# Kernel tuning notes

Measured on AMD Instinct MI355X. Metric: run time of the kernel, lower is better.

## Reference

```python
import jax, jax.numpy as jnp
import numpy as np
from jax import lax


def conv2d(x, w, b=None, pad=0):
    y = lax.conv_general_dilated(x, w, (1, 1), [(pad, pad), (pad, pad)],
                                 dimension_numbers=('NCHW', 'OIHW', 'NCHW'))
    if b is not None:
        y = y + b[None, :, None, None]
    return y


def setup_inputs():
    key = jax.random.key(0)
    ks = jax.random.split(key, 8)
    B, C, H, W = 8, 3, 224, 224
    OC, NH, HD = 32, 8, 4
    s = lambda fan: 1.0 / np.sqrt(fan)
    x = jax.random.normal(ks[0], (B, C, H, W), jnp.float32)
    # gumbel noise for the hard gumbel-softmax over attention logits [B,NH,HD,H,H]
    gumbel = jax.random.gumbel(ks[1], (B, NH, HD, H, H), jnp.float32)
    in_w = jax.random.normal(ks[2], (OC, C, 3, 3), jnp.float32) * s(C * 9)
    in_b = jnp.zeros((OC,), jnp.float32)
    qkv_w = jax.random.normal(ks[3], (3 * OC, OC, 3, 3), jnp.float32) * s(OC * 9)
    proj_w = jax.random.normal(ks[4], (OC, OC, 1, 1), jnp.float32) * s(OC)
    proj_b = jnp.zeros((OC,), jnp.float32)
    upd_w = jax.random.normal(ks[5], (OC, OC, 1, 1), jnp.float32) * s(OC)
    upd_b = jnp.zeros((OC,), jnp.float32)
    bn_gamma = jnp.ones((OC,), jnp.float32)
    bn_beta = jnp.zeros((OC,), jnp.float32)
    return {"x": x, "gumbel": gumbel, "in_w": in_w, "in_b": in_b, "qkv_w": qkv_w,
            "proj_w": proj_w, "proj_b": proj_b, "upd_w": upd_w, "upd_b": upd_b,
            "bn_gamma": bn_gamma, "bn_beta": bn_beta}


def reference(x, gumbel, in_w, in_b, qkv_w, proj_w, proj_b, upd_w, upd_b, bn_gamma, bn_beta):
    B, _, H, W = x.shape
    NH, HD = 8, 4
    OC = NH * HD
    EPS = 1e-5
    x1 = conv2d(x, in_w, in_b, pad=1)                       # [B,32,H,W]
    qkv = conv2d(x1, qkv_w, None, pad=1).reshape(B, NH, 3, HD, H, W)
    q, k, v = qkv[:, :, 0], qkv[:, :, 1], qkv[:, :, 2]      # each [B,NH,HD,H,W]
    scale = HD ** -0.5
    # matmul(q, k^T) over the last two dims -> [B,NH,HD,H,H]
    logits = jnp.einsum('bndiw,bndjw->bndij', q, k) * scale
    # hard gumbel-softmax, tau=1, straight-through
    y_soft = jax.nn.softmax(logits + gumbel, axis=-1)
    idx = jnp.argmax(y_soft, axis=-1)
    y_hard = jax.nn.one_hot(idx, H, dtype=y_soft.dtype)
    att = y_hard - lax.stop_gradient(y_soft) + y_soft
    A = jnp.einsum('bndij,bndjw->bndiw', att, v).reshape(B, OC, H, W)
    # F.interpolate to (224,224) bilinear is identity since H=W=224
    A = conv2d(A, proj_w, proj_b)
    A = conv2d(A, upd_w, upd_b)
    # BatchNorm2d in training mode (batch statistics, biased variance)
    mean = A.mean(axis=(0, 2, 3), keepdims=True)
    var = ((A - mean) ** 2).mean(axis=(0, 2, 3), keepdims=True)
    A = (A - mean) * lax.rsqrt(var + EPS)
    A = A * bn_gamma[None, :, None, None] + bn_beta[None, :, None, None]
    A = A * jax.nn.sigmoid(A)  # SiLU; dropout is identity (eval)
    out = A + x1
    return out, att
```

## Files before the change

### kernel.cpp

```cpp
#include <hip/hip_runtime.h>
#include <hip/hip_bf16.h>

#define NB 8
#define CIN 3
#define HH 224
#define WW 224
#define OC 32
#define NH 8
#define HD 4
#define NHD 32
#define C96 96
#define HWSZ (HH*WW)

#define PH 226
#define PW 228
#define CHS (PH*PW)

#define HT 4
#define OCT 8
#define NGB 4


__device__ __forceinline__ void gld_lds16(const float* gsrc, float* ldst) {
    __builtin_amdgcn_global_load_lds(
        (const __attribute__((address_space(1))) uint32_t*)gsrc,
        (__attribute__((address_space(3))) uint32_t*)ldst,
        16, 0, 0);
}

__global__ void k_w2(const float* __restrict__ pw, const float* __restrict__ pb,
                     const float* __restrict__ uw, const float* __restrict__ ub,
                     float* __restrict__ W2, float* __restrict__ b2) {
    int c = threadIdx.x, o = threadIdx.y;
    float acc = 0.f;
    for (int m = 0; m < OC; ++m) acc = fmaf(uw[o*OC + m], pw[m*OC + c], acc);
    W2[o*OC + c] = acc;
    if (c == 0) {
        float bb = ub[o];
        for (int m = 0; m < OC; ++m) bb = fmaf(uw[o*OC + m], pb[m], bb);
        b2[o] = bb;
    }
}

__global__ __launch_bounds__(256) void k_conv_in_tile(const float* __restrict__ x,
                                                      const float* __restrict__ w,
                                                      const float* __restrict__ bias,
                                                      float* __restrict__ x1) {
    int h0 = blockIdx.x * 2;
    int b  = blockIdx.y;
    __shared__ float xs[CIN][4][226];
    int t = threadIdx.x;
    for (int ch = 0; ch < CIN; ++ch)
        for (int r = 0; r < 4; ++r) {
            int gh = h0 - 1 + r;
            for (int col = t; col < 226; col += 256) {
                float v = 0.f;
                if (gh >= 0 && gh < HH && col > 0 && col < 225)
                    v = x[((size_t)(b*CIN + ch)*HH + gh)*WW + (col-1)];
                xs[ch][r][col] = v;
            }
        }
    __syncthreads();
    int wv = t;
    if (wv >= WW) return;
    float xv[CIN][4][3];
    #pragma unroll
    for (int c = 0; c < CIN; ++c)
        #pragma unroll
        for (int r = 0; r < 4; ++r)
            #pragma unroll
            for (int j = 0; j < 3; ++j)
                xv[c][r][j] = xs[c][r][wv + j];
    float acc[2][OC];
    #pragma unroll
    for (int hy = 0; hy < 2; ++hy)
        for (int oc = 0; oc < OC; ++oc) acc[hy][oc] = 0.f;
    #pragma unroll
    for (int c = 0; c < CIN; ++c)
        #pragma unroll
        for (int kh = 0; kh < 3; ++kh)
            #pragma unroll
            for (int kw = 0; kw < 3; ++kw)
                for (int oc = 0; oc < OC; ++oc) {
                    float wgt = w[oc*CIN*9 + c*9 + kh*3 + kw];
                    #pragma unroll
                    for (int hy = 0; hy < 2; ++hy)
                        acc[hy][oc] = fmaf(xv[c][hy+kh][kw], wgt, acc[hy][oc]);
                }
    for (int oc = 0; oc < OC; ++oc) {
        float bs = bias[oc];
        #pragma unroll
        for (int hy = 0; hy < 2; ++hy)
            x1[((size_t)(b*OC + oc)*PH + (h0+hy+1))*PW + (wv+1)] = __fadd_rn(acc[hy][oc], bs);
    }
}

__global__ __launch_bounds__(256) void k_conv_qkv_tile(const float* __restrict__ x1g,
                                                       const float* __restrict__ w,
                                                       float* __restrict__ qk4,
                                                       float* __restrict__ vbg) {
    int h0 = blockIdx.x * HT;
    int og = blockIdx.y * OCT;
    int z  = blockIdx.z;
    const float* x1b = x1g + (size_t)z*OC*CHS;
    float* qk = qk4 + (size_t)z*64*HWSZ;
    float* vb = vbg + (size_t)z*OC*HWSZ;
    __shared__ float xs[2][2240];
    int t = threadIdx.x;
    int lane = t & 63, wid = t >> 6;
    int wv = t;
    float acc[HT][OCT];
    #pragma unroll
    for (int a = 0; a < HT; ++a)
        #pragma unroll
        for (int o = 0; o < OCT; ++o) acc[a][o] = 0.f;

    {
        const float* src = x1b + (size_t)h0*PW;
        for (int k = wid; k < 6; k += 4)
            gld_lds16(src + k*256 + lane*4, &xs[0][k*256]);
    }
    __syncthreads();

    for (int c = 0; c < OC; ++c) {
        int cur = c & 1;
        if (c + 1 < OC) {
            const float* src = x1b + (size_t)(c+1)*CHS + (size_t)h0*PW;
            float* dst = xs[cur ^ 1];
            for (int k = wid; k < 6; k += 4)
                gld_lds16(src + k*256 + lane*4, dst + k*256);
        }
        if (wv < WW) {
            float xv[HT+2][3];
            #pragma unroll
            for (int r = 0; r < HT+2; ++r)
                #pragma unroll
                for (int j = 0; j < 3; ++j)
                    xv[r][j] = xs[cur][r*PW + wv + j];
            #pragma unroll
            for (int o = 0; o < OCT; ++o) {
                const float* wr = w + ((size_t)(og + o)*OC + c)*9;
                #pragma unroll
                for (int kh = 0; kh < 3; ++kh)
                    #pragma unroll
                    for (int kw = 0; kw < 3; ++kw) {
                        float wgt = wr[kh*3 + kw];
                        #pragma unroll
                        for (int hy = 0; hy < HT; ++hy)
                            acc[hy][o] = fmaf(xv[hy+kh][kw], wgt, acc[hy][o]);
                    }
            }
        }
        __syncthreads();
    }
    if (wv < WW) {
        #pragma unroll
        for (int o = 0; o < OCT; ++o) {
            int oc = og + o;
            int rem = oc % 12;
            int r = rem >> 2, d = rem & 3;
            int n = oc / 12;
            if (r == 0) {
                #pragma unroll
                for (int hy = 0; hy < HT; ++hy)
                    qk[((size_t)(n*8 + d)*HH + (h0+hy))*WW + wv] = acc[hy][o];
            } else if (r == 2) {
                #pragma unroll
                for (int hy = 0; hy < HT; ++hy)
                    vb[((size_t)(n*4 + d)*HH + (h0+hy))*WW + wv] = acc[hy][o];
            }
        }
    }
    int ogm = og % 12;
    if (ogm != 8) {
        int ko = (ogm == 0) ? 4 : 0;
        int n  = og / 12;
        float* kt = &xs[0][0];
        if (wv < WW) {
            int wb = wv >> 2, wl = wv & 3;
            #pragma unroll
            for (int kk = 0; kk < 4; ++kk)
                #pragma unroll
                for (int hy = 0; hy < HT; ++hy)
                    kt[(kk*56 + wb)*20 + hy*4 + wl] = acc[hy][ko + kk];
        }
        __syncthreads();
        if (wv < WW) {
            int wb = wv >> 2, s = wv & 3;
            #pragma unroll
            for (int kk = 0; kk < 4; ++kk) {
                float4 kvv = *(const float4*)(&kt[(kk*56 + wb)*20 + s*4]);
                *(float4*)(qk + (size_t)(n*8 + 4 + kk)*HWSZ
                               + (size_t)wb*(HH*4) + (size_t)(h0 + s)*4) = kvv;
            }
        }
    }
}

__global__ __launch_bounds__(256) void k_attn_ri(const float* __restrict__ qk4,
                                                 const float* __restrict__ gum,
                                                 float* __restrict__ att,
                                                 int* __restrict__ idxout,
                                                 int b0) {
    int i0 = blockIdx.x * 8;
    int nd = blockIdx.y;
    int z  = blockIdx.z;
    int b  = b0 + z;
    const float* qkz = qk4 + (size_t)z*64*HWSZ;
    const float* gumb = gum + (size_t)b*NHD*HH*HH;
    float* attb = att + (size_t)b*NHD*HH*HH;
    int* idxb = idxout + (size_t)b*NHD*HH;
    int n = nd >> 2, d = nd & 3;
    const float* qb = qkz + ((size_t)(n*8 + d)*HH + i0)*WW;
    const float* kT = qkz + (size_t)(n*8 + 4 + d)*HWSZ;
    __shared__ __align__(16) float qs[8][WW];
    __shared__ float vals[8][256];
    __shared__ int   win_s[8];
    int t = threadIdx.x;
    for (int f = t; f < 8*(WW/4); f += 256) {
        int r = f / (WW/4), p = (f % (WW/4))*4;
        *(float4*)(&qs[r][p]) = *(const float4*)(qb + (size_t)r*WW + p);
    }
    __syncthreads();
    if (t < WW) {
        float s0[8], s1[8], s2[8], s3[8];
        #pragma unroll
        for (int ii = 0; ii < 8; ++ii) { s0[ii]=0.f; s1[ii]=0.f; s2[ii]=0.f; s3[ii]=0.f; }
        const float* kTt = kT + (size_t)t*4;
        for (int w = 0; w < WW; w += 4) {
            float4 kc = *(const float4*)(kTt + (size_t)(w >> 2)*(HH*4));
            #pragma unroll
            for (int ii = 0; ii < 8; ++ii) {
                float4 qc = *(const float4*)(&qs[ii][w]);
                s0[ii] = __fadd_rn(s0[ii], __fmul_rn(qc.x, kc.x));
                s1[ii] = __fadd_rn(s1[ii], __fmul_rn(qc.y, kc.y));
                s2[ii] = __fadd_rn(s2[ii], __fmul_rn(qc.z, kc.z));
                s3[ii] = __fadd_rn(s3[ii], __fmul_rn(qc.w, kc.w));
            }
        }
        #pragma unroll
        for (int ii = 0; ii < 8; ++ii) {
            float dot = __fadd_rn(__fadd_rn(s0[ii], s1[ii]), __fadd_rn(s2[ii], s3[ii]));
            vals[ii][t] = __fadd_rn(__fmul_rn(0.5f, dot),
                                    gumb[((size_t)nd*HH + (i0 + ii))*HH + t]);
        }
    } else {
        #pragma unroll
        for (int ii = 0; ii < 8; ++ii) vals[ii][t] = -INFINITY;
    }
    __syncthreads();
    int ii = t >> 5, jj = t & 31;
    float best = -INFINITY; int bj = 0x7fffffff;
    for (int j = jj; j < 256; j += 32) {
        float v = vals[ii][j];
        if (v > best) { best = v; bj = j; }
    }
    for (int off = 16; off > 0; off >>= 1) {
        float v2 = __shfl_down(best, off, 32);
        int   j2 = __shfl_down(bj,   off, 32);
        if (v2 > best || (v2 == best && j2 < bj)) { best = v2; bj = j2; }
    }
    if (jj == 0) { win_s[ii] = bj; idxb[nd*HH + i0 + ii] = bj; }
    __syncthreads();
    for (int e = t; e < 8*WW; e += 256) {
        int r = e / WW, j = e - r*WW;
        attb[((size_t)nd*HH + (i0 + r))*HH + j] = (j == win_s[r]) ? 1.f : 0.f;
    }
}

__global__ __launch_bounds__(256) void k_gather_mm(const float* __restrict__ vbuf,
                                                   const int* __restrict__ idx,
                                                   const float* __restrict__ W2g,
                                                   const float* __restrict__ b2g,
                                                   float* __restrict__ A2) {
    int i = blockIdx.x, b = blockIdx.y;
    __shared__ float w2s[OC*OC];
    __shared__ float b2s[OC];
    __shared__ int   id[OC];
    for (int t = threadIdx.x; t < OC*OC; t += blockDim.x) w2s[t] = W2g[t];
    if (threadIdx.x < OC) {
        b2s[threadIdx.x] = b2g[threadIdx.x];
        id[threadIdx.x]  = idx[(b*NHD + threadIdx.x)*HH + i];
    }
    __syncthreads();
    int wv = threadIdx.x;
    if (wv >= WW) return;
    float vals[OC];
    for (int c = 0; c < OC; ++c)
        vals[c] = vbuf[((size_t)(b*OC + c)*HH + id[c])*WW + wv];
    for (int oc = 0; oc < OC; ++oc) {
        float a = b2s[oc];
        for (int c = 0; c < OC; ++c) a = fmaf(w2s[oc*OC + c], vals[c], a);
        A2[((size_t)(b*OC + oc)*HH + i)*WW + wv] = a;
    }
}

__global__ __launch_bounds__(256) void k_stats(const float* __restrict__ A2,
                                               float* __restrict__ sums,
                                               float* __restrict__ sumsq) {
    int oc = blockIdx.x, s = blockIdx.y;
    int t = threadIdx.x;
    float a = 0.f, a2 = 0.f;
    const int SL = HWSZ/16;
    for (int b = 0; b < NB; ++b) {
        const float* base = A2 + (size_t)(b*OC + oc)*HWSZ + s*SL;
        for (int e = t*4; e < SL; e += 256*4) {
            float4 v = *(const float4*)(base + e);
            a  += v.x + v.y + v.z + v.w;
            a2 += v.x*v.x + v.y*v.y + v.z*v.z + v.w*v.w;
        }
    }
    __shared__ float r1[256], r2[256];
    r1[t] = a; r2[t] = a2;
    __syncthreads();
    for (int st = 128; st > 0; st >>= 1) {
        if (t < st) { r1[t] += r1[t+st]; r2[t] += r2[t+st]; }
        __syncthreads();
    }
    if (t == 0) { atomicAdd(&sums[oc], r1[0]); atomicAdd(&sumsq[oc], r2[0]); }
}

__global__ __launch_bounds__(256) void k_final(const float* __restrict__ A2,
                                               const float* __restrict__ x1,
                                               const float* __restrict__ sums,
                                               const float* __restrict__ sumsq,
                                               const float* __restrict__ gamma,
                                               const float* __restrict__ beta,
                                               float* __restrict__ out) {
    int i = blockIdx.x, b = blockIdx.y;
    __shared__ float mean_s[OC], inv_s[OC], g_s[OC], be_s[OC];
    if (threadIdx.x < OC) {
        int oc = threadIdx.x;
        const float N = (float)(NB*HH*WW);
        float mean = sums[oc]/N;
        float var  = sumsq[oc]/N - mean*mean;
        mean_s[oc] = mean;
        inv_s[oc]  = rsqrtf(var + 1e-5f);
        g_s[oc]    = gamma[oc];
        be_s[oc]   = beta[oc];
    }
    __syncthreads();
    int wv = threadIdx.x;
    if (wv >= WW) return;
    for (int oc = 0; oc < OC; ++oc) {
        size_t o = ((size_t)(b*OC + oc)*HH + i)*WW + wv;
        float a = A2[o];
        float an = (a - mean_s[oc])*inv_s[oc]*g_s[oc] + be_s[oc];
        float sw = an / (1.f + __expf(-an));
        out[o] = sw + x1[((size_t)(b*OC + oc)*PH + (i+1))*PW + (wv+1)];
    }
}

extern "C" void kernel_launch(void* const* d_in, const int* in_sizes, int n_in,
                              void* d_out, int out_size, void* d_ws, size_t ws_size,
                              hipStream_t stream) {
    const float* x      = (const float*)d_in[0];
    const float* gumbel = (const float*)d_in[1];
    const float* in_w   = (const float*)d_in[2];
    const float* in_b   = (const float*)d_in[3];
    const float* qkv_w  = (const float*)d_in[4];
    const float* proj_w = (const float*)d_in[5];
    const float* proj_b = (const float*)d_in[6];
    const float* upd_w  = (const float*)d_in[7];
    const float* upd_b  = (const float*)d_in[8];
    const float* bng    = (const float*)d_in[9];
    const float* bnb    = (const float*)d_in[10];

    float* out = (float*)d_out;
    float* att = out + (size_t)NB*OC*HWSZ;

    float* x1   = (float*)d_ws;
    float* qk4  = x1 + (size_t)NB*OC*CHS;
    float* A2   = qk4;
    float* vbuf = qk4 + (size_t)NGB*64*HWSZ;
    float* W2   = vbuf + (size_t)NB*OC*HWSZ;
    float* b2   = W2 + OC*OC;
    float* sums = b2 + OC;
    float* sumsq= sums + OC;
    int*   idx  = (int*)(sumsq + OC);

    hipMemsetAsync(x1, 0, (size_t)NB*OC*CHS*sizeof(float), stream);
    hipMemsetAsync(sums, 0, 2*OC*sizeof(float), stream);

    k_w2          <<<1, dim3(OC, OC), 0, stream>>>(proj_w, proj_b, upd_w, upd_b, W2, b2);
    k_conv_in_tile<<<dim3(HH/2, NB), 256, 0, stream>>>(x, in_w, in_b, x1);

    for (int g = 0; g < NB/NGB; ++g) {
        k_conv_qkv_tile<<<dim3(HH/HT, C96/OCT, NGB), 256, 0, stream>>>(
            x1 + (size_t)g*NGB*OC*CHS, qkv_w, qk4, vbuf + (size_t)g*NGB*OC*HWSZ);
        k_attn_ri<<<dim3(HH/8, NHD, NGB), 256, 0, stream>>>(
            qk4, gumbel, att, idx, g*NGB);
    }

    k_gather_mm<<<dim3(HH, NB), 256, 0, stream>>>(vbuf, idx, W2, b2, A2);
    k_stats    <<<dim3(OC, 16), 256, 0, stream>>>(A2, sums, sumsq);
    k_final    <<<dim3(HH, NB), 256, 0, stream>>>(A2, x1, sums, sumsq, bng, bnb, out);
}
```

Before: 746.7 us.

## Stage two channels per sync in qkv conv; memset att and scatter one-hot ones

The qkv convolution now double-buffers two input channels per pipeline step, which halves the number of barriers and gives each load more time to overlap with compute. The attention kernel no longer writes the full one-hot row. Instead the att buffer is zeroed with a hipMemsetAsync up front and each row gets a single 1.0 store at the argmax. This swaps per-element conditional stores for a bulk memset, but the whole att tensor (~51 MB) is still written once by the memset.

```diff
diff --git a/kernel.cpp b/kernel.cpp
--- a/kernel.cpp
+++ b/kernel.cpp
@@ -105,7 +105,7 @@
     const float* x1b = x1g + (size_t)z*OC*CHS;
     float* qk = qk4 + (size_t)z*64*HWSZ;
     float* vb = vbg + (size_t)z*OC*HWSZ;
-    __shared__ float xs[2][2240];
+    __shared__ float xs[2][3072];
     int t = threadIdx.x;
     int lane = t & 63, wid = t >> 6;
     int wv = t;
@@ -115,40 +115,47 @@
         #pragma unroll
         for (int o = 0; o < OCT; ++o) acc[a][o] = 0.f;
 
-    {
-        const float* src = x1b + (size_t)h0*PW;
+    #pragma unroll
+    for (int cc = 0; cc < 2; ++cc) {
+        const float* src = x1b + (size_t)cc*CHS + (size_t)h0*PW;
         for (int k = wid; k < 6; k += 4)
-            gld_lds16(src + k*256 + lane*4, &xs[0][k*256]);
-    }
-    __syncthreads();
-
-    for (int c = 0; c < OC; ++c) {
-        int cur = c & 1;
-        if (c + 1 < OC) {
-            const float* src = x1b + (size_t)(c+1)*CHS + (size_t)h0*PW;
+            gld_lds16(src + k*256 + lane*4, &xs[0][cc*1536 + k*256]);
+    }
+    __syncthreads();
+
+    for (int p = 0; p < OC/2; ++p) {
+        int cur = p & 1;
+        if (p + 1 < OC/2) {
             float* dst = xs[cur ^ 1];
-            for (int k = wid; k < 6; k += 4)
-                gld_lds16(src + k*256 + lane*4, dst + k*256);
+            #pragma unroll
+            for (int cc = 0; cc < 2; ++cc) {
+                const float* src = x1b + (size_t)((p+1)*2 + cc)*CHS + (size_t)h0*PW;
+                for (int k = wid; k < 6; k += 4)
+                    gld_lds16(src + k*256 + lane*4, dst + cc*1536 + k*256);
+            }
         }
         if (wv < WW) {
-            float xv[HT+2][3];
-            #pragma unroll
-            for (int r = 0; r < HT+2; ++r)
+            for (int cc = 0; cc < 2; ++cc) {
+                int c = p*2 + cc;
+                float xv[HT+2][3];
                 #pragma unroll
-                for (int j = 0; j < 3; ++j)
-                    xv[r][j] = xs[cur][r*PW + wv + j];
-            #pragma unroll
-            for (int o = 0; o < OCT; ++o) {
-                const float* wr = w + ((size_t)(og + o)*OC + c)*9;
+                for (int r = 0; r < HT+2; ++r)
+                    #pragma unroll
+                    for (int j = 0; j < 3; ++j)
+                        xv[r][j] = xs[cur][cc*1536 + r*PW + wv + j];
                 #pragma unroll
-                for (int kh = 0; kh < 3; ++kh)
+                for (int o = 0; o < OCT; ++o) {
+                    const float* wr = w + ((size_t)(og + o)*OC + c)*9;
                     #pragma unroll
-                    for (int kw = 0; kw < 3; ++kw) {
-                        float wgt = wr[kh*3 + kw];
+                    for (int kh = 0; kh < 3; ++kh)
                         #pragma unroll
-                        for (int hy = 0; hy < HT; ++hy)
-                            acc[hy][o] = fmaf(xv[hy+kh][kw], wgt, acc[hy][o]);
-                    }
+                        for (int kw = 0; kw < 3; ++kw) {
+                            float wgt = wr[kh*3 + kw];
+                            #pragma unroll
+                            for (int hy = 0; hy < HT; ++hy)
+                                acc[hy][o] = fmaf(xv[hy+kh][kw], wgt, acc[hy][o]);
+                        }
+                }
             }
         }
         __syncthreads();
@@ -176,6 +183,7 @@
         int ko = (ogm == 0) ? 4 : 0;
         int n  = og / 12;
         float* kt = &xs[0][0];
+        __syncthreads();
         if (wv < WW) {
             int wb = wv >> 2, wl = wv & 3;
             #pragma unroll
@@ -215,7 +223,6 @@
     const float* kT = qkz + (size_t)(n*8 + 4 + d)*HWSZ;
     __shared__ __align__(16) float qs[8][WW];
     __shared__ float vals[8][256];
-    __shared__ int   win_s[8];
     int t = threadIdx.x;
     for (int f = t; f < 8*(WW/4); f += 256) {
         int r = f / (WW/4), p = (f % (WW/4))*4;
@@ -260,11 +267,9 @@
         int   j2 = __shfl_down(bj,   off, 32);
         if (v2 > best || (v2 == best && j2 < bj)) { best = v2; bj = j2; }
     }
-    if (jj == 0) { win_s[ii] = bj; idxb[nd*HH + i0 + ii] = bj; }
-    __syncthreads();
-    for (int e = t; e < 8*WW; e += 256) {
-        int r = e / WW, j = e - r*WW;
-        attb[((size_t)nd*HH + (i0 + r))*HH + j] = (j == win_s[r]) ? 1.f : 0.f;
+    if (jj == 0) {
+        idxb[nd*HH + i0 + ii] = bj;
+        attb[((size_t)nd*HH + (i0 + ii))*HH + bj] = 1.f;
     }
 }
 
@@ -380,6 +385,7 @@
     int*   idx  = (int*)(sumsq + OC);
 
     hipMemsetAsync(x1, 0, (size_t)NB*OC*CHS*sizeof(float), stream);
+    hipMemsetAsync(att, 0, (size_t)NB*NHD*HH*HH*sizeof(float), stream);
     hipMemsetAsync(sums, 0, 2*OC*sizeof(float), stream);
 
     k_w2          <<<1, dim3(OC, OC), 0, stream>>>(proj_w, proj_b, upd_w, upd_b, W2, b2);
```

Measured after the change: 791.5 us. 6.0% more time.

## Restructure attention argmax kernel to one wavefront with register tiling and memset

Applied to the files above, without the earlier changes.

The attention-row kernel now runs one 64-thread wavefront per block covering 4 query rows, with each thread computing a 4x4 register tile of dot products (4 keys by 4 rows). This raises reuse of each K load and removes the shared-memory staging and block-level syncs. The argmax becomes a full-wavefront shuffle reduction. The dense one-hot output is no longer written element by element; it is zeroed with a memset and only the winning entry is set. This trades register pressure and a larger memset for less store traffic and fewer barriers, though only 56 of the 64 lanes do useful work.

```diff
diff --git a/kernel.cpp b/kernel.cpp
--- a/kernel.cpp
+++ b/kernel.cpp
@@ -197,12 +197,12 @@
     }
 }
 
-__global__ __launch_bounds__(256) void k_attn_ri(const float* __restrict__ qk4,
-                                                 const float* __restrict__ gum,
-                                                 float* __restrict__ att,
-                                                 int* __restrict__ idxout,
-                                                 int b0) {
-    int i0 = blockIdx.x * 8;
+__global__ __launch_bounds__(64) void k_attn_ri(const float* __restrict__ qk4,
+                                                const float* __restrict__ gum,
+                                                float* __restrict__ att,
+                                                int* __restrict__ idxout,
+                                                int b0) {
+    int i0 = blockIdx.x * 4;
     int nd = blockIdx.y;
     int z  = blockIdx.z;
     int b  = b0 + z;
@@ -212,59 +212,74 @@
     int* idxb = idxout + (size_t)b*NHD*HH;
     int n = nd >> 2, d = nd & 3;
     const float* qb = qkz + ((size_t)(n*8 + d)*HH + i0)*WW;
-    const float* kT = qkz + (size_t)(n*8 + 4 + d)*HWSZ;
-    __shared__ __align__(16) float qs[8][WW];
-    __shared__ float vals[8][256];
-    __shared__ int   win_s[8];
+    const float4* kT4 = (const float4*)(qkz + (size_t)(n*8 + 4 + d)*HWSZ);
+    __shared__ __align__(16) float qs[4*WW];
     int t = threadIdx.x;
-    for (int f = t; f < 8*(WW/4); f += 256) {
-        int r = f / (WW/4), p = (f % (WW/4))*4;
-        *(float4*)(&qs[r][p]) = *(const float4*)(qb + (size_t)r*WW + p);
-    }
-    __syncthreads();
-    if (t < WW) {
-        float s0[8], s1[8], s2[8], s3[8];
-        #pragma unroll
-        for (int ii = 0; ii < 8; ++ii) { s0[ii]=0.f; s1[ii]=0.f; s2[ii]=0.f; s3[ii]=0.f; }
-        const float* kTt = kT + (size_t)t*4;
-        for (int w = 0; w < WW; w += 4) {
-            float4 kc = *(const float4*)(kTt + (size_t)(w >> 2)*(HH*4));
-            #pragma unroll
-            for (int ii = 0; ii < 8; ++ii) {
-                float4 qc = *(const float4*)(&qs[ii][w]);
-                s0[ii] = __fadd_rn(s0[ii], __fmul_rn(qc.x, kc.x));
-                s1[ii] = __fadd_rn(s1[ii], __fmul_rn(qc.y, kc.y));
-                s2[ii] = __fadd_rn(s2[ii], __fmul_rn(qc.z, kc.z));
-                s3[ii] = __fadd_rn(s3[ii], __fmul_rn(qc.w, kc.w));
-            }
-        }
-        #pragma unroll
-        for (int ii = 0; ii < 8; ++ii) {
-            float dot = __fadd_rn(__fadd_rn(s0[ii], s1[ii]), __fadd_rn(s2[ii], s3[ii]));
-            vals[ii][t] = __fadd_rn(__fmul_rn(0.5f, dot),
-                                    gumb[((size_t)nd*HH + (i0 + ii))*HH + t]);
+    for (int f = t; f < 4*(WW/4); f += 64)
+        *(float4*)(&qs[f*4]) = *(const float4*)(qb + (size_t)f*4);
+    __syncthreads();
+
+    float s0[4][4], s1[4][4], s2[4][4], s3[4][4];
+    #pragma unroll
+    for (int jj = 0; jj < 4; ++jj)
+        #pragma unroll
+        for (int ii = 0; ii < 4; ++ii)
+            { s0[jj][ii]=0.f; s1[jj][ii]=0.f; s2[jj][ii]=0.f; s3[jj][ii]=0.f; }
+
+    for (int w = 0; w < WW; w += 4) {
+        int wb = w >> 2;
+        float4 kc[4];
+        #pragma unroll
+        for (int jj = 0; jj < 4; ++jj)
+            kc[jj] = kT4[(size_t)wb*224 + 4*t + jj];
+        #pragma unroll
+        for (int ii = 0; ii < 4; ++ii) {
+            float4 qc = *(const float4*)(&qs[ii*WW + w]);
+            #pragma unroll
+            for (int jj = 0; jj < 4; ++jj) {
+                s0[jj][ii] = __fadd_rn(s0[jj][ii], __fmul_rn(qc.x, kc[jj].x));
+                s1[jj][ii] = __fadd_rn(s1[jj][ii], __fmul_rn(qc.y, kc[jj].y));
+                s2[jj][ii] = __fadd_rn(s2[jj][ii], __fmul_rn(qc.z, kc[jj].z));
+                s3[jj][ii] = __fadd_rn(s3[jj][ii], __fmul_rn(qc.w, kc[jj].w));
+            }
+        }
+    }
+
+    float v[4][4];
+    if (t < 56) {
+        #pragma unroll
+        for (int ii = 0; ii < 4; ++ii) {
+            float4 gc = *(const float4*)(gumb + ((size_t)nd*HH + (i0+ii))*HH + 4*t);
+            #pragma unroll
+            for (int jj = 0; jj < 4; ++jj) {
+                float dot = __fadd_rn(__fadd_rn(s0[jj][ii], s1[jj][ii]),
+                                      __fadd_rn(s2[jj][ii], s3[jj][ii]));
+                float g = (jj==0)?gc.x:(jj==1)?gc.y:(jj==2)?gc.z:gc.w;
+                v[ii][jj] = __fadd_rn(__fmul_rn(0.5f, dot), g);
+            }
         }
     } else {
         #pragma unroll
-        for (int ii = 0; ii < 8; ++ii) vals[ii][t] = -INFINITY;
-    }
-    __syncthreads();
-    int ii = t >> 5, jj = t & 31;
-    float best = -INFINITY; int bj = 0x7fffffff;
-    for (int j = jj; j < 256; j += 32) {
-        float v = vals[ii][j];
-        if (v > best) { best = v; bj = j; }
-    }
-    for (int off = 16; off > 0; off >>= 1) {
-        float v2 = __shfl_down(best, off, 32);
-        int   j2 = __shfl_down(bj,   off, 32);
-        if (v2 > best || (v2 == best && j2 < bj)) { best = v2; bj = j2; }
-    }
-    if (jj == 0) { win_s[ii] = bj; idxb[nd*HH + i0 + ii] = bj; }
-    __syncthreads();
-    for (int e = t; e < 8*WW; e += 256) {
-        int r = e / WW, j = e - r*WW;
-        attb[((size_t)nd*HH + (i0 + r))*HH + j] = (j == win_s[r]) ? 1.f : 0.f;
+        for (int ii = 0; ii < 4; ++ii)
+            #pragma unroll
+            for (int jj = 0; jj < 4; ++jj) v[ii][jj] = -INFINITY;
+    }
+
+    #pragma unroll
+    for (int ii = 0; ii < 4; ++ii) {
+        float best = v[ii][0]; int bj = (t < 56) ? 4*t : 0x7fffffff;
+        #pragma unroll
+        for (int jj = 1; jj < 4; ++jj)
+            if (v[ii][jj] > best) { best = v[ii][jj]; bj = 4*t + jj; }
+        for (int off = 32; off > 0; off >>= 1) {
+            float v2 = __shfl_down(best, off, 64);
+            int   j2 = __shfl_down(bj,   off, 64);
+            if (v2 > best || (v2 == best && j2 < bj)) { best = v2; bj = j2; }
+        }
+        if (t == 0) {
+            idxb[nd*HH + i0 + ii] = bj;
+            attb[((size_t)nd*HH + (i0 + ii))*HH + bj] = 1.f;
+        }
     }
 }
 
@@ -380,6 +395,7 @@
     int*   idx  = (int*)(sumsq + OC);
 
     hipMemsetAsync(x1, 0, (size_t)NB*OC*CHS*sizeof(float), stream);
+    hipMemsetAsync(att, 0, (size_t)NB*NHD*HH*HH*sizeof(float), stream);
     hipMemsetAsync(sums, 0, 2*OC*sizeof(float), stream);
 
     k_w2          <<<1, dim3(OC, OC), 0, stream>>>(proj_w, proj_b, upd_w, upd_b, W2, b2);
@@ -388,7 +404,7 @@
     for (int g = 0; g < NB/NGB; ++g) {
         k_conv_qkv_tile<<<dim3(HH/HT, C96/OCT, NGB), 256, 0, stream>>>(
             x1 + (size_t)g*NGB*OC*CHS, qkv_w, qk4, vbuf + (size_t)g*NGB*OC*HWSZ);
-        k_attn_ri<<<dim3(HH/8, NHD, NGB), 256, 0, stream>>>(
+        k_attn_ri<<<dim3(HH/4, NHD, NGB), 64, 0, stream>>>(
             qk4, gumbel, att, idx, g*NGB);
     }
 
```

After: 854.3 us. +14.4%, slower.
